# Performance work log

Hardware: AMD Instinct MI355X
Metric: run time of the kernel (lower is better)

Reference implementation:

```python
import jax, jax.numpy as jnp
import numpy as np

B, S, D, H, F, E = 8, 1024, 1024, 16, 3584, 2
HD = D // H
NUM_LABELS = 2
EPS = 1e-6


def setup_inputs() -> dict:
    key = jax.random.key(0)
    ks = jax.random.split(key, 10)
    w = lambda k, shape: jax.random.normal(k, shape, jnp.float32) * 0.02
    return {
        "hidden_states": jax.random.normal(ks[0], (B, S, D), jnp.float32),
        "ln1_w": jnp.ones((D,), jnp.float32),
        "q_w": w(ks[1], (D, D)),
        "k_w": w(ks[2], (D, D)),
        "v_w": w(ks[3], (D, D)),
        "o_w": w(ks[4], (D, D)),
        "ln2_w": jnp.ones((D,), jnp.float32),
        "router_w": w(ks[5], (D, E)),
        "gate_w": w(ks[6], (E, D, F)),
        "up_w": w(ks[7], (E, D, F)),
        "down_w": w(ks[8], (E, F, D)),
        "final_ln_w": jnp.ones((D,), jnp.float32),
        "score_w": w(ks[9], (D, NUM_LABELS)),
    }


def rmsnorm(x, w):
    var = jnp.mean(jnp.square(x), axis=-1, keepdims=True)
    return x * jax.lax.rsqrt(var + EPS) * w


def reference(hidden_states, ln1_w, q_w, k_w, v_w, o_w, ln2_w, router_w,
              gate_w, up_w, down_w, final_ln_w, score_w):
    x = hidden_states  # [B,S,D]
    # --- attention block (Jamba attention: no RoPE, no bias, causal) ---
    res = x
    h = rmsnorm(x, ln1_w)
    q = (h @ q_w).reshape(B, S, H, HD).transpose(0, 2, 1, 3)  # [B,H,S,HD]
    k = (h @ k_w).reshape(B, S, H, HD).transpose(0, 2, 1, 3)
    v = (h @ v_w).reshape(B, S, H, HD).transpose(0, 2, 1, 3)
    scores = jnp.einsum("bhqd,bhkd->bhqk", q, k) / np.sqrt(HD).astype(np.float32)
    causal = jnp.tril(jnp.ones((S, S), bool))
    scores = jnp.where(causal, scores, jnp.finfo(jnp.float32).min)
    attn = jax.nn.softmax(scores, axis=-1)
    ctx = jnp.einsum("bhqk,bhkd->bhqd", attn, v)
    attn_out = ctx.transpose(0, 2, 1, 3).reshape(B, S, D) @ o_w
    x = res + attn_out
    # --- top-1 MoE FFN (Jamba: softmax router, top-k, NO renormalization) ---
    res = x
    h = rmsnorm(x, ln2_w).reshape(B * S, D)
    router_logits = h @ router_w  # [N,E]
    probs = jax.nn.softmax(router_logits.astype(jnp.float32), axis=-1)
    top_w = jnp.max(probs, axis=-1)       # top-1 weight
    sel = jnp.argmax(probs, axis=-1)      # selected expert id
    moe = jnp.zeros_like(h)
    for e in range(E):  # fixed tiny loop over experts
        y = (jax.nn.silu(h @ gate_w[e]) * (h @ up_w[e])) @ down_w[e]
        moe = moe + jnp.where(sel == e, top_w, 0.0)[:, None] * y
    x = res + moe.reshape(B, S, D)
    # --- final RMSNorm + score head on first token ---
    x = rmsnorm(x, final_ln_w)
    logits = x[:, 0, :] @ score_w  # [B, NUM_LABELS]
    return logits
```

## Files before the change

kernel.cpp:

```cpp
#include <hip/hip_runtime.h>
#include <math.h>

#define B 8
#define S 1024
#define D 1024
#define F 3584

#define NBLK 256
#define KSV 64
#define CHV 16
#define KS5 16
#define CH5 64
#define KS6 112
#define CH6 32

#define LD4(p) (*(const float4*)(p))
#define FMA4(A, s, W) { (A).x += (s)*(W).x; (A).y += (s)*(W).y; (A).z += (s)*(W).z; (A).w += (s)*(W).w; }

#define BB8(bb, ACC, XS, CH, koff) { \
  float4 xa = LD4((XS) + (bb)*(CH) + (koff)); \
  float4 xb = LD4((XS) + (bb)*(CH) + (koff) + 4); \
  FMA4(ACC, xa.x, w0); FMA4(ACC, xa.y, w1); FMA4(ACC, xa.z, w2); FMA4(ACC, xa.w, w3); \
  FMA4(ACC, xb.x, w4); FMA4(ACC, xb.y, w5); FMA4(ACC, xb.z, w6); FMA4(ACC, xb.w, w7); }

#define ALL8(XS, CH, koff) \
  BB8(0, acc0, XS, CH, koff) BB8(1, acc1, XS, CH, koff) \
  BB8(2, acc2, XS, CH, koff) BB8(3, acc3, XS, CH, koff) \
  BB8(4, acc4, XS, CH, koff) BB8(5, acc5, XS, CH, koff) \
  BB8(6, acc6, XS, CH, koff) BB8(7, acc7, XS, CH, koff)

__device__ __forceinline__ float block_sum256(float v, volatile float* buf) {
  #pragma unroll
  for (int o = 32; o; o >>= 1) v += __shfl_down(v, o);
  __syncthreads();
  if ((threadIdx.x & 63) == 0) buf[threadIdx.x >> 6] = v;
  __syncthreads();
  return buf[0] + buf[1] + buf[2] + buf[3];
}

__device__ __forceinline__ void gsync(unsigned* bar, int phase) {
  __syncthreads();
  if (threadIdx.x == 0) {
    unsigned* flag = bar + 32 * phase;
    unsigned old = __hip_atomic_fetch_add(bar, 1u, __ATOMIC_ACQ_REL,
                                          __HIP_MEMORY_SCOPE_AGENT);
    if (old == (unsigned)(NBLK * phase) - 1u) {
      __hip_atomic_store(flag, 1u, __ATOMIC_RELEASE, __HIP_MEMORY_SCOPE_AGENT);
    } else {
      while (__hip_atomic_load(flag, __ATOMIC_RELAXED,
                               __HIP_MEMORY_SCOPE_AGENT) == 0u)
        __builtin_amdgcn_s_sleep(8);
      (void)__hip_atomic_load(flag, __ATOMIC_ACQUIRE, __HIP_MEMORY_SCOPE_AGENT);
    }
  }
  __syncthreads();
}

__device__ __forceinline__ void mv16(const float4* __restrict__ Wp,
                                     float* __restrict__ Pout,
                                     const float* xs, int j) {
  const int st = D / 4;
  float4 acc0 = {0,0,0,0}, acc1 = {0,0,0,0}, acc2 = {0,0,0,0}, acc3 = {0,0,0,0};
  float4 acc4 = {0,0,0,0}, acc5 = {0,0,0,0}, acc6 = {0,0,0,0}, acc7 = {0,0,0,0};
  float4 w0 = Wp[0*st], w1 = Wp[1*st], w2 = Wp[2*st], w3 = Wp[3*st];
  float4 w4 = Wp[4*st], w5 = Wp[5*st], w6 = Wp[6*st], w7 = Wp[7*st];
  float4 v0 = Wp[8*st], v1 = Wp[9*st], v2 = Wp[10*st], v3 = Wp[11*st];
  float4 v4 = Wp[12*st], v5 = Wp[13*st], v6 = Wp[14*st], v7 = Wp[15*st];
  ALL8(xs, CHV, 0);
  w0 = v0; w1 = v1; w2 = v2; w3 = v3; w4 = v4; w5 = v5; w6 = v6; w7 = v7;
  ALL8(xs, CHV, 8);
  *(float4*)(Pout + 0*(size_t)D + j) = acc0;
  *(float4*)(Pout + 1*(size_t)D + j) = acc1;
  *(float4*)(Pout + 2*(size_t)D + j) = acc2;
  *(float4*)(Pout + 3*(size_t)D + j) = acc3;
  *(float4*)(Pout + 4*(size_t)D + j) = acc4;
  *(float4*)(Pout + 5*(size_t)D + j) = acc5;
  *(float4*)(Pout + 6*(size_t)D + j) = acc6;
  *(float4*)(Pout + 7*(size_t)D + j) = acc7;
}

__global__ __launch_bounds__(256, 1) void k_fused(
    const float* __restrict__ hs, const float* __restrict__ ln1,
    const float* __restrict__ vw, const float* __restrict__ ow,
    const float* __restrict__ ln2, const float* __restrict__ rw,
    const float* __restrict__ gw, const float* __restrict__ uw,
    const float* __restrict__ dw, const float* __restrict__ flw,
    const float* __restrict__ sw, float* __restrict__ out,
    float* __restrict__ wsf, unsigned* __restrict__ bar) {
  __shared__ float xs[512];
  __shared__ float rbuf[4];
  const int tid = threadIdx.x;
  const int bid = blockIdx.x;

  float* h1    = wsf;
  float* Vp    = wsf + 8192;
  float* Op    = Vp + (size_t)KSV * 8 * D;
  float* xr    = Op + (size_t)KSV * 8 * D;
  float* h2    = xr + 8192;
  float* tw8   = h2 + 8192;
  int*   sel8  = (int*)(tw8 + 8);
  float* Pgu   = tw8 + 16;
  float* Dp    = Pgu + (size_t)KS5 * 4 * 8 * F;
  float* dummy = Dp + (size_t)KS6 * 2 * 8 * D;

  if (bid < 8) {
    int idx = tid * 4;
    float4 x = LD4(hs + (size_t)bid * S * D + idx);
    float ss = x.x*x.x + x.y*x.y + x.z*x.z + x.w*x.w;
    float tot = block_sum256(ss, rbuf);
    float sc = rsqrtf(tot * (1.f / (float)D) + 1e-6f);
    float4 wv = LD4(ln1 + idx);
    float4 o;
    o.x = x.x*sc*wv.x; o.y = x.y*sc*wv.y; o.z = x.z*sc*wv.z; o.w = x.w*sc*wv.w;
    *(float4*)(h1 + bid * D + idx) = o;
  }
  gsync(bar, 1);

  float4 pref = {0,0,0,0};

  if (bid < KSV) {
    int i0 = bid * CHV;
    if (tid < 128) xs[tid] = h1[(tid >> 4) * D + i0 + (tid & 15)];
    __syncthreads();
    int j = tid * 4;
    mv16((const float4*)(vw + (size_t)i0 * D + j), Vp + (size_t)bid * 8 * D, xs, j);
  } else {
    const float4* src = (const float4*)gw + (size_t)(bid - 64) * 4096 + tid;
    #pragma unroll
    for (int t = 0; t < 16; t++) {
      float4 v = src[(size_t)t * 256];
      pref.x += v.x; pref.y += v.y; pref.z += v.z; pref.w += v.w;
    }
  }
  gsync(bar, 2);

  if (bid < KSV) {
    int i0 = bid * CHV;
    if (tid < 128) {
      int bb = tid >> 4, ii = tid & 15;
      float s = 0.f;
      #pragma unroll 8
      for (int p = 0; p < KSV; p++) s += Vp[((size_t)p * 8 + bb) * D + i0 + ii];
      xs[bb * 16 + ii] = s;
    }
    __syncthreads();
    int j = tid * 4;
    mv16((const float4*)(ow + (size_t)i0 * D + j), Op + (size_t)bid * 8 * D, xs, j);
  } else {
    const float4* src = (const float4*)uw + (size_t)(bid - 64) * 4096 + tid;
    #pragma unroll
    for (int t = 0; t < 16; t++) {
      float4 v = src[(size_t)t * 256];
      pref.x += v.x; pref.y += v.y; pref.z += v.z; pref.w += v.w;
    }
    float tchk = pref.x + pref.y + pref.z + pref.w;
    if (tchk > 1e30f) dummy[bid] = tchk;
  }
  gsync(bar, 3);

  if (bid < 8) {
    int idx = tid * 4;
    float4 x = LD4(hs + (size_t)bid * S * D + idx);
    #pragma unroll 8
    for (int p = 0; p < KSV; p++) {
      float4 v = LD4(Op + ((size_t)p * 8 + bid) * D + idx);
      x.x += v.x; x.y += v.y; x.z += v.z; x.w += v.w;
    }
    *(float4*)(xr + bid * D + idx) = x;
    float ss = x.x*x.x + x.y*x.y + x.z*x.z + x.w*x.w;
    float tot = block_sum256(ss, rbuf);
    float sc = rsqrtf(tot * (1.f / (float)D) + 1e-6f);
    float4 wv = LD4(ln2 + idx);
    float4 h;
    h.x = x.x*sc*wv.x; h.y = x.y*sc*wv.y; h.z = x.z*sc*wv.z; h.w = x.w*sc*wv.w;
    *(float4*)(h2 + bid * D + idx) = h;
    float r0 = h.x * rw[idx * 2]     + h.y * rw[(idx + 1) * 2] +
               h.z * rw[(idx + 2) * 2] + h.w * rw[(idx + 3) * 2];
    float r1 = h.x * rw[idx * 2 + 1]     + h.y * rw[(idx + 1) * 2 + 1] +
               h.z * rw[(idx + 2) * 2 + 1] + h.w * rw[(idx + 3) * 2 + 1];
    r0 = block_sum256(r0, rbuf);
    r1 = block_sum256(r1, rbuf);
    if (tid == 0) {
      float m = fmaxf(r0, r1);
      float e0 = __expf(r0 - m), e1 = __expf(r1 - m);
      float inv = 1.f / (e0 + e1);
      float p0 = e0 * inv, p1 = e1 * inv;
      tw8[bid] = fmaxf(p0, p1);
      sel8[bid] = (p1 > p0) ? 1 : 0;
    }
  }
  gsync(bar, 4);

  if (bid < 14 * KS5) {
    int kc = bid & 15, colt = bid >> 4;
    int i0 = kc * CH5;
    { int bb = tid >> 6, r = tid & 63;
      xs[tid]       = h2[bb * D + i0 + r];
      xs[tid + 256] = h2[(bb + 4) * D + i0 + r]; }
    __syncthreads();
    int c = colt * 1024 + tid * 4;
    int m = c / F;
    int j = c - m * F;
    const float* base = (m < 2 ? gw : uw) + (size_t)(m & 1) * D * F;
    const float4* Wp = (const float4*)(base + (size_t)i0 * F + j);
    const int st = F / 4;
    float4 acc0 = {0,0,0,0}, acc1 = {0,0,0,0}, acc2 = {0,0,0,0}, acc3 = {0,0,0,0};
    float4 acc4 = {0,0,0,0}, acc5 = {0,0,0,0}, acc6 = {0,0,0,0}, acc7 = {0,0,0,0};
    float4 w0 = Wp[0*st], w1 = Wp[1*st], w2 = Wp[2*st], w3 = Wp[3*st];
    float4 w4 = Wp[4*st], w5 = Wp[5*st], w6 = Wp[6*st], w7 = Wp[7*st];
    Wp += 8 * st;
    #pragma unroll
    for (int t = 0; t < CH5 / 8 - 1; t++) {
      float4 n0 = Wp[0*st], n1 = Wp[1*st], n2 = Wp[2*st], n3 = Wp[3*st];
      float4 n4 = Wp[4*st], n5 = Wp[5*st], n6 = Wp[6*st], n7 = Wp[7*st];
      Wp += 8 * st;
      ALL8(xs, CH5, t * 8);
      w0 = n0; w1 = n1; w2 = n2; w3 = n3; w4 = n4; w5 = n5; w6 = n6; w7 = n7;
    }
    ALL8(xs, CH5, CH5 - 8);
    #define GU_ST(bb, ACC) \
      *(float4*)(Pgu + (((size_t)kc * 4 + m) * 8 + (bb)) * F + j) = ACC;
    GU_ST(0, acc0) GU_ST(1, acc1) GU_ST(2, acc2) GU_ST(3, acc3)
    GU_ST(4, acc4) GU_ST(5, acc5) GU_ST(6, acc6) GU_ST(7, acc7)
    #undef GU_ST
  }
  gsync(bar, 5);

  if (bid < 2 * KS6) {
    int e = bid & 1, ch = bid >> 1, i0 = ch * CH6;
    { int bb = tid >> 5, ii = tid & 31;
      float ga = 0.f, ua = 0.f;
      #pragma unroll
      for (int kc = 0; kc < KS5; kc++) {
        ga += Pgu[(((size_t)kc * 4 + e)     * 8 + bb) * F + i0 + ii];
        ua += Pgu[(((size_t)kc * 4 + 2 + e) * 8 + bb) * F + i0 + ii];
      }
      xs[bb * CH6 + ii] = (ga / (1.f + __expf(-ga))) * ua; }
    __syncthreads();
    int j = tid * 4;
    const float4* Wp = (const float4*)(dw + (size_t)e * F * D + (size_t)i0 * D + j);
    const int st = D / 4;
    float4 acc0 = {0,0,0,0}, acc1 = {0,0,0,0}, acc2 = {0,0,0,0}, acc3 = {0,0,0,0};
    float4 acc4 = {0,0,0,0}, acc5 = {0,0,0,0}, acc6 = {0,0,0,0}, acc7 = {0,0,0,0};
    float4 w0 = Wp[0*st], w1 = Wp[1*st], w2 = Wp[2*st], w3 = Wp[3*st];
    float4 w4 = Wp[4*st], w5 = Wp[5*st], w6 = Wp[6*st], w7 = Wp[7*st];
    Wp += 8 * st;
    #pragma unroll
    for (int t = 0; t < CH6 / 8 - 1; t++) {
      float4 n0 = Wp[0*st], n1 = Wp[1*st], n2 = Wp[2*st], n3 = Wp[3*st];
      float4 n4 = Wp[4*st], n5 = Wp[5*st], n6 = Wp[6*st], n7 = Wp[7*st];
      Wp += 8 * st;
      ALL8(xs, CH6, t * 8);
      w0 = n0; w1 = n1; w2 = n2; w3 = n3; w4 = n4; w5 = n5; w6 = n6; w7 = n7;
    }
    ALL8(xs, CH6, CH6 - 8);
    #define DN_ST(bb, ACC) \
      *(float4*)(Dp + (((size_t)ch * 2 + e) * 8 + (bb)) * D + j) = ACC;
    DN_ST(0, acc0) DN_ST(1, acc1) DN_ST(2, acc2) DN_ST(3, acc3)
    DN_ST(4, acc4) DN_ST(5, acc5) DN_ST(6, acc6) DN_ST(7, acc7)
    #undef DN_ST
  }
  gsync(bar, 6);

  if (bid < 8) {
    int e = sel8[bid];
    float tw = tw8[bid];
    int idx = tid * 4;
    float4 y = {0,0,0,0};
    #pragma unroll 8
    for (int p = 0; p < KS6; p++) {
      float4 v = LD4(Dp + (((size_t)p * 2 + e) * 8 + bid) * D + idx);
      y.x += v.x; y.y += v.y; y.z += v.z; y.w += v.w;
    }
    float4 x = LD4(xr + bid * D + idx);
    x.x += tw * y.x; x.y += tw * y.y; x.z += tw * y.z; x.w += tw * y.w;
    float ss = x.x*x.x + x.y*x.y + x.z*x.z + x.w*x.w;
    float tot = block_sum256(ss, rbuf);
    float sc = rsqrtf(tot * (1.f / (float)D) + 1e-6f);
    float4 wv = LD4(flw + idx);
    float n0 = x.x*sc*wv.x, n1 = x.y*sc*wv.y, n2 = x.z*sc*wv.z, n3 = x.w*sc*wv.w;
    float l0 = n0 * sw[idx * 2]     + n1 * sw[(idx + 1) * 2] +
               n2 * sw[(idx + 2) * 2] + n3 * sw[(idx + 3) * 2];
    float l1 = n0 * sw[idx * 2 + 1]     + n1 * sw[(idx + 1) * 2 + 1] +
               n2 * sw[(idx + 2) * 2 + 1] + n3 * sw[(idx + 3) * 2 + 1];
    l0 = block_sum256(l0, rbuf);
    l1 = block_sum256(l1, rbuf);
    if (tid == 0) { out[bid * 2 + 0] = l0; out[bid * 2 + 1] = l1; }
  }
}

extern "C" void kernel_launch(void* const* d_in, const int* in_sizes, int n_in,
                              void* d_out, int out_size, void* d_ws, size_t ws_size,
                              hipStream_t stream) {
  const float* hs  = (const float*)d_in[0];
  const float* ln1 = (const float*)d_in[1];
  const float* vw  = (const float*)d_in[4];
  const float* ow  = (const float*)d_in[5];
  const float* ln2 = (const float*)d_in[6];
  const float* rw  = (const float*)d_in[7];
  const float* gw  = (const float*)d_in[8];
  const float* uw  = (const float*)d_in[9];
  const float* dw  = (const float*)d_in[10];
  const float* flw = (const float*)d_in[11];
  const float* sw  = (const float*)d_in[12];

  unsigned* bar = (unsigned*)d_ws;
  float* wsf = (float*)d_ws + 256;

  (void)hipMemsetAsync(d_ws, 0, 1024, stream);
  hipLaunchKernelGGL(k_fused, dim3(NBLK), dim3(256), 0, stream,
                     hs, ln1, vw, ow, ln2, rw, gw, uw, dw, flw, sw,
                     (float*)d_out, wsf, bar);
}
```

Baseline: 252.2 us.

## Split persistent grid-synced kernel into six separate launches

Replaces the single persistent kernel with hand-rolled atomic grid barriers by six kernels launched back to back on the stream. The idle-block weight prefetch of gate/up weights is dropped, and RMSNorm-1 is folded into the V projection kernel. Gate/up and down kernels now skip storing partial results for experts a row did not select. The change trades barrier spin costs for kernel-launch gaps and loses the L2 prefetch overlap.

```diff
diff --git a/kernel.cpp b/kernel.cpp
--- a/kernel.cpp
+++ b/kernel.cpp
@@ -6,7 +6,6 @@
 #define D 1024
 #define F 3584
 
-#define NBLK 256
 #define KSV 64
 #define CHV 16
 #define KS5 16
@@ -36,24 +35,6 @@
   if ((threadIdx.x & 63) == 0) buf[threadIdx.x >> 6] = v;
   __syncthreads();
   return buf[0] + buf[1] + buf[2] + buf[3];
-}
-
-__device__ __forceinline__ void gsync(unsigned* bar, int phase) {
-  __syncthreads();
-  if (threadIdx.x == 0) {
-    unsigned* flag = bar + 32 * phase;
-    unsigned old = __hip_atomic_fetch_add(bar, 1u, __ATOMIC_ACQ_REL,
-                                          __HIP_MEMORY_SCOPE_AGENT);
-    if (old == (unsigned)(NBLK * phase) - 1u) {
-      __hip_atomic_store(flag, 1u, __ATOMIC_RELEASE, __HIP_MEMORY_SCOPE_AGENT);
-    } else {
-      while (__hip_atomic_load(flag, __ATOMIC_RELAXED,
-                               __HIP_MEMORY_SCOPE_AGENT) == 0u)
-        __builtin_amdgcn_s_sleep(8);
-      (void)__hip_atomic_load(flag, __ATOMIC_ACQUIRE, __HIP_MEMORY_SCOPE_AGENT);
-    }
-  }
-  __syncthreads();
 }
 
 __device__ __forceinline__ void mv16(const float4* __restrict__ Wp,
@@ -79,214 +60,215 @@
   *(float4*)(Pout + 7*(size_t)D + j) = acc7;
 }
 
-__global__ __launch_bounds__(256, 1) void k_fused(
-    const float* __restrict__ hs, const float* __restrict__ ln1,
-    const float* __restrict__ vw, const float* __restrict__ ow,
-    const float* __restrict__ ln2, const float* __restrict__ rw,
-    const float* __restrict__ gw, const float* __restrict__ uw,
-    const float* __restrict__ dw, const float* __restrict__ flw,
-    const float* __restrict__ sw, float* __restrict__ out,
-    float* __restrict__ wsf, unsigned* __restrict__ bar) {
-  __shared__ float xs[512];
-  __shared__ float rbuf[4];
-  const int tid = threadIdx.x;
-  const int bid = blockIdx.x;
-
-  float* h1    = wsf;
-  float* Vp    = wsf + 8192;
-  float* Op    = Vp + (size_t)KSV * 8 * D;
-  float* xr    = Op + (size_t)KSV * 8 * D;
-  float* h2    = xr + 8192;
-  float* tw8   = h2 + 8192;
-  int*   sel8  = (int*)(tw8 + 8);
-  float* Pgu   = tw8 + 16;
-  float* Dp    = Pgu + (size_t)KS5 * 4 * 8 * F;
-  float* dummy = Dp + (size_t)KS6 * 2 * 8 * D;
-
-  if (bid < 8) {
-    int idx = tid * 4;
-    float4 x = LD4(hs + (size_t)bid * S * D + idx);
-    float ss = x.x*x.x + x.y*x.y + x.z*x.z + x.w*x.w;
-    float tot = block_sum256(ss, rbuf);
-    float sc = rsqrtf(tot * (1.f / (float)D) + 1e-6f);
-    float4 wv = LD4(ln1 + idx);
-    float4 o;
-    o.x = x.x*sc*wv.x; o.y = x.y*sc*wv.y; o.z = x.z*sc*wv.z; o.w = x.w*sc*wv.w;
-    *(float4*)(h1 + bid * D + idx) = o;
-  }
-  gsync(bar, 1);
-
-  float4 pref = {0,0,0,0};
-
-  if (bid < KSV) {
-    int i0 = bid * CHV;
-    if (tid < 128) xs[tid] = h1[(tid >> 4) * D + i0 + (tid & 15)];
-    __syncthreads();
-    int j = tid * 4;
-    mv16((const float4*)(vw + (size_t)i0 * D + j), Vp + (size_t)bid * 8 * D, xs, j);
-  } else {
-    const float4* src = (const float4*)gw + (size_t)(bid - 64) * 4096 + tid;
+__global__ __launch_bounds__(256, 2) void k_mvp_v(const float* __restrict__ hs,
+                                                  const float* __restrict__ ln1w,
+                                                  const float* __restrict__ vw,
+                                                  float* __restrict__ Vp) {
+  __shared__ float xs[8 * CHV];
+  __shared__ float scsh[8];
+  int tid = threadIdx.x;
+  int w = tid >> 6, lane = tid & 63;
+  #pragma unroll
+  for (int b2 = 0; b2 < 2; b2++) {
+    int b = w * 2 + b2;
+    const float4* hp = (const float4*)(hs + (size_t)b * S * D);
+    float ss = 0.f;
     #pragma unroll
-    for (int t = 0; t < 16; t++) {
-      float4 v = src[(size_t)t * 256];
-      pref.x += v.x; pref.y += v.y; pref.z += v.z; pref.w += v.w;
+    for (int t = 0; t < 4; t++) {
+      float4 v = hp[lane * 4 + t];
+      ss += v.x*v.x + v.y*v.y + v.z*v.z + v.w*v.w;
     }
-  }
-  gsync(bar, 2);
-
-  if (bid < KSV) {
-    int i0 = bid * CHV;
-    if (tid < 128) {
-      int bb = tid >> 4, ii = tid & 15;
-      float s = 0.f;
-      #pragma unroll 8
-      for (int p = 0; p < KSV; p++) s += Vp[((size_t)p * 8 + bb) * D + i0 + ii];
-      xs[bb * 16 + ii] = s;
-    }
-    __syncthreads();
-    int j = tid * 4;
-    mv16((const float4*)(ow + (size_t)i0 * D + j), Op + (size_t)bid * 8 * D, xs, j);
-  } else {
-    const float4* src = (const float4*)uw + (size_t)(bid - 64) * 4096 + tid;
     #pragma unroll
-    for (int t = 0; t < 16; t++) {
-      float4 v = src[(size_t)t * 256];
-      pref.x += v.x; pref.y += v.y; pref.z += v.z; pref.w += v.w;
-    }
-    float tchk = pref.x + pref.y + pref.z + pref.w;
-    if (tchk > 1e30f) dummy[bid] = tchk;
-  }
-  gsync(bar, 3);
-
-  if (bid < 8) {
-    int idx = tid * 4;
-    float4 x = LD4(hs + (size_t)bid * S * D + idx);
-    #pragma unroll 8
-    for (int p = 0; p < KSV; p++) {
-      float4 v = LD4(Op + ((size_t)p * 8 + bid) * D + idx);
-      x.x += v.x; x.y += v.y; x.z += v.z; x.w += v.w;
-    }
-    *(float4*)(xr + bid * D + idx) = x;
-    float ss = x.x*x.x + x.y*x.y + x.z*x.z + x.w*x.w;
-    float tot = block_sum256(ss, rbuf);
-    float sc = rsqrtf(tot * (1.f / (float)D) + 1e-6f);
-    float4 wv = LD4(ln2 + idx);
-    float4 h;
-    h.x = x.x*sc*wv.x; h.y = x.y*sc*wv.y; h.z = x.z*sc*wv.z; h.w = x.w*sc*wv.w;
-    *(float4*)(h2 + bid * D + idx) = h;
-    float r0 = h.x * rw[idx * 2]     + h.y * rw[(idx + 1) * 2] +
-               h.z * rw[(idx + 2) * 2] + h.w * rw[(idx + 3) * 2];
-    float r1 = h.x * rw[idx * 2 + 1]     + h.y * rw[(idx + 1) * 2 + 1] +
-               h.z * rw[(idx + 2) * 2 + 1] + h.w * rw[(idx + 3) * 2 + 1];
-    r0 = block_sum256(r0, rbuf);
-    r1 = block_sum256(r1, rbuf);
-    if (tid == 0) {
-      float m = fmaxf(r0, r1);
-      float e0 = __expf(r0 - m), e1 = __expf(r1 - m);
-      float inv = 1.f / (e0 + e1);
-      float p0 = e0 * inv, p1 = e1 * inv;
-      tw8[bid] = fmaxf(p0, p1);
-      sel8[bid] = (p1 > p0) ? 1 : 0;
-    }
-  }
-  gsync(bar, 4);
-
-  if (bid < 14 * KS5) {
-    int kc = bid & 15, colt = bid >> 4;
-    int i0 = kc * CH5;
-    { int bb = tid >> 6, r = tid & 63;
-      xs[tid]       = h2[bb * D + i0 + r];
-      xs[tid + 256] = h2[(bb + 4) * D + i0 + r]; }
-    __syncthreads();
-    int c = colt * 1024 + tid * 4;
-    int m = c / F;
-    int j = c - m * F;
-    const float* base = (m < 2 ? gw : uw) + (size_t)(m & 1) * D * F;
-    const float4* Wp = (const float4*)(base + (size_t)i0 * F + j);
-    const int st = F / 4;
-    float4 acc0 = {0,0,0,0}, acc1 = {0,0,0,0}, acc2 = {0,0,0,0}, acc3 = {0,0,0,0};
-    float4 acc4 = {0,0,0,0}, acc5 = {0,0,0,0}, acc6 = {0,0,0,0}, acc7 = {0,0,0,0};
-    float4 w0 = Wp[0*st], w1 = Wp[1*st], w2 = Wp[2*st], w3 = Wp[3*st];
-    float4 w4 = Wp[4*st], w5 = Wp[5*st], w6 = Wp[6*st], w7 = Wp[7*st];
+    for (int o = 32; o; o >>= 1) ss += __shfl_down(ss, o);
+    if (lane == 0) scsh[b] = rsqrtf(ss * (1.f / (float)D) + 1e-6f);
+  }
+  __syncthreads();
+  int i0 = blockIdx.x * CHV;
+  if (tid < 128) {
+    int bb = tid >> 4, ii = tid & 15;
+    xs[tid] = hs[(size_t)bb * S * D + i0 + ii] * scsh[bb] * ln1w[i0 + ii];
+  }
+  __syncthreads();
+  int j = tid * 4;
+  mv16((const float4*)(vw + (size_t)i0 * D + j), Vp + (size_t)blockIdx.x * 8 * D, xs, j);
+}
+
+__global__ __launch_bounds__(256, 2) void k_ored(const float* __restrict__ Vp,
+                                                 const float* __restrict__ ow,
+                                                 float* __restrict__ Op) {
+  __shared__ float xs[8 * CHV];
+  int tid = threadIdx.x;
+  int i0 = blockIdx.x * CHV;
+  if (tid < 128) {
+    int bb = tid >> 4, ii = tid & 15;
+    float s = 0.f;
+    #pragma unroll 16
+    for (int p = 0; p < KSV; p++) s += Vp[((size_t)p * 8 + bb) * D + i0 + ii];
+    xs[bb * CHV + ii] = s;
+  }
+  __syncthreads();
+  int j = tid * 4;
+  mv16((const float4*)(ow + (size_t)i0 * D + j), Op + (size_t)blockIdx.x * 8 * D, xs, j);
+}
+
+__global__ void k_mid(const float* __restrict__ hs, const float* __restrict__ Op,
+                      const float* __restrict__ ln2, const float* __restrict__ rw,
+                      float* __restrict__ xr, float* __restrict__ h2,
+                      float* __restrict__ topw, int* __restrict__ sel) {
+  __shared__ float buf[4];
+  int b = blockIdx.x;
+  int idx = threadIdx.x * 4;
+  float4 x = LD4(hs + (size_t)b * S * D + idx);
+  #pragma unroll 16
+  for (int p = 0; p < KSV; p++) {
+    float4 v = LD4(Op + ((size_t)p * 8 + b) * D + idx);
+    x.x += v.x; x.y += v.y; x.z += v.z; x.w += v.w;
+  }
+  *(float4*)(xr + b * D + idx) = x;
+  float ss = x.x*x.x + x.y*x.y + x.z*x.z + x.w*x.w;
+  float tot = block_sum256(ss, buf);
+  float sc = rsqrtf(tot * (1.f / (float)D) + 1e-6f);
+  float4 wv = LD4(ln2 + idx);
+  float4 h;
+  h.x = x.x*sc*wv.x; h.y = x.y*sc*wv.y; h.z = x.z*sc*wv.z; h.w = x.w*sc*wv.w;
+  *(float4*)(h2 + b * D + idx) = h;
+  float r0 = h.x * rw[idx * 2]     + h.y * rw[(idx + 1) * 2] +
+             h.z * rw[(idx + 2) * 2] + h.w * rw[(idx + 3) * 2];
+  float r1 = h.x * rw[idx * 2 + 1]     + h.y * rw[(idx + 1) * 2 + 1] +
+             h.z * rw[(idx + 2) * 2 + 1] + h.w * rw[(idx + 3) * 2 + 1];
+  r0 = block_sum256(r0, buf);
+  r1 = block_sum256(r1, buf);
+  if (threadIdx.x == 0) {
+    float m = fmaxf(r0, r1);
+    float e0 = __expf(r0 - m), e1 = __expf(r1 - m);
+    float inv = 1.f / (e0 + e1);
+    float p0 = e0 * inv, p1 = e1 * inv;
+    topw[b] = fmaxf(p0, p1);
+    sel[b] = (p1 > p0) ? 1 : 0;
+  }
+}
+
+__global__ __launch_bounds__(256, 2) void k_gateup(const float* __restrict__ h2,
+                                                   const float* __restrict__ gw,
+                                                   const float* __restrict__ uw,
+                                                   const int* __restrict__ sel,
+                                                   float* __restrict__ Pgu) {
+  __shared__ float xs[8 * CH5];
+  __shared__ int ssel[8];
+  int tid = threadIdx.x;
+  int kc = blockIdx.y, colt = blockIdx.x;
+  int i0 = kc * CH5;
+  { int bb = tid >> 6, r = tid & 63;
+    xs[tid]       = h2[bb * D + i0 + r];
+    xs[tid + 256] = h2[(bb + 4) * D + i0 + r]; }
+  if (tid < 8) ssel[tid] = sel[tid];
+  __syncthreads();
+  int c = colt * 1024 + tid * 4;
+  int m = c / F;
+  int j = c - m * F;
+  const float* base = (m < 2 ? gw : uw) + (size_t)(m & 1) * D * F;
+  const float4* Wp = (const float4*)(base + (size_t)i0 * F + j);
+  const int st = F / 4;
+  float4 acc0 = {0,0,0,0}, acc1 = {0,0,0,0}, acc2 = {0,0,0,0}, acc3 = {0,0,0,0};
+  float4 acc4 = {0,0,0,0}, acc5 = {0,0,0,0}, acc6 = {0,0,0,0}, acc7 = {0,0,0,0};
+  float4 w0 = Wp[0*st], w1 = Wp[1*st], w2 = Wp[2*st], w3 = Wp[3*st];
+  float4 w4 = Wp[4*st], w5 = Wp[5*st], w6 = Wp[6*st], w7 = Wp[7*st];
+  Wp += 8 * st;
+  #pragma unroll
+  for (int t = 0; t < CH5 / 8 - 1; t++) {
+    float4 n0 = Wp[0*st], n1 = Wp[1*st], n2 = Wp[2*st], n3 = Wp[3*st];
+    float4 n4 = Wp[4*st], n5 = Wp[5*st], n6 = Wp[6*st], n7 = Wp[7*st];
     Wp += 8 * st;
-    #pragma unroll
-    for (int t = 0; t < CH5 / 8 - 1; t++) {
-      float4 n0 = Wp[0*st], n1 = Wp[1*st], n2 = Wp[2*st], n3 = Wp[3*st];
-      float4 n4 = Wp[4*st], n5 = Wp[5*st], n6 = Wp[6*st], n7 = Wp[7*st];
-      Wp += 8 * st;
-      ALL8(xs, CH5, t * 8);
-      w0 = n0; w1 = n1; w2 = n2; w3 = n3; w4 = n4; w5 = n5; w6 = n6; w7 = n7;
-    }
-    ALL8(xs, CH5, CH5 - 8);
-    #define GU_ST(bb, ACC) \
+    ALL8(xs, CH5, t * 8);
+    w0 = n0; w1 = n1; w2 = n2; w3 = n3; w4 = n4; w5 = n5; w6 = n6; w7 = n7;
+  }
+  ALL8(xs, CH5, CH5 - 8);
+  int me = m & 1;
+  #define GU_ST(bb, ACC) \
+    if (ssel[bb] == me) \
       *(float4*)(Pgu + (((size_t)kc * 4 + m) * 8 + (bb)) * F + j) = ACC;
-    GU_ST(0, acc0) GU_ST(1, acc1) GU_ST(2, acc2) GU_ST(3, acc3)
-    GU_ST(4, acc4) GU_ST(5, acc5) GU_ST(6, acc6) GU_ST(7, acc7)
-    #undef GU_ST
-  }
-  gsync(bar, 5);
-
-  if (bid < 2 * KS6) {
-    int e = bid & 1, ch = bid >> 1, i0 = ch * CH6;
-    { int bb = tid >> 5, ii = tid & 31;
+  GU_ST(0, acc0) GU_ST(1, acc1) GU_ST(2, acc2) GU_ST(3, acc3)
+  GU_ST(4, acc4) GU_ST(5, acc5) GU_ST(6, acc6) GU_ST(7, acc7)
+  #undef GU_ST
+}
+
+__global__ __launch_bounds__(256, 2) void k_down(const float* __restrict__ Pgu,
+                                                 const float* __restrict__ dw,
+                                                 const int* __restrict__ sel,
+                                                 float* __restrict__ Dp) {
+  __shared__ float xs[8 * CH6];
+  __shared__ int ssel[8];
+  int tid = threadIdx.x;
+  int e = blockIdx.x & 1, ch = blockIdx.x >> 1, i0 = ch * CH6;
+  if (tid < 8) ssel[tid] = sel[tid];
+  __syncthreads();
+  { int bb = tid >> 5, ii = tid & 31;
+    float r = 0.f;
+    if (ssel[bb] == e) {
       float ga = 0.f, ua = 0.f;
       #pragma unroll
       for (int kc = 0; kc < KS5; kc++) {
         ga += Pgu[(((size_t)kc * 4 + e)     * 8 + bb) * F + i0 + ii];
         ua += Pgu[(((size_t)kc * 4 + 2 + e) * 8 + bb) * F + i0 + ii];
       }
-      xs[bb * CH6 + ii] = (ga / (1.f + __expf(-ga))) * ua; }
-    __syncthreads();
-    int j = tid * 4;
-    const float4* Wp = (const float4*)(dw + (size_t)e * F * D + (size_t)i0 * D + j);
-    const int st = D / 4;
-    float4 acc0 = {0,0,0,0}, acc1 = {0,0,0,0}, acc2 = {0,0,0,0}, acc3 = {0,0,0,0};
-    float4 acc4 = {0,0,0,0}, acc5 = {0,0,0,0}, acc6 = {0,0,0,0}, acc7 = {0,0,0,0};
-    float4 w0 = Wp[0*st], w1 = Wp[1*st], w2 = Wp[2*st], w3 = Wp[3*st];
-    float4 w4 = Wp[4*st], w5 = Wp[5*st], w6 = Wp[6*st], w7 = Wp[7*st];
+      r = (ga / (1.f + __expf(-ga))) * ua;
+    }
+    xs[bb * CH6 + ii] = r; }
+  __syncthreads();
+  int j = tid * 4;
+  const float4* Wp = (const float4*)(dw + (size_t)e * F * D + (size_t)i0 * D + j);
+  const int st = D / 4;
+  float4 acc0 = {0,0,0,0}, acc1 = {0,0,0,0}, acc2 = {0,0,0,0}, acc3 = {0,0,0,0};
+  float4 acc4 = {0,0,0,0}, acc5 = {0,0,0,0}, acc6 = {0,0,0,0}, acc7 = {0,0,0,0};
+  float4 w0 = Wp[0*st], w1 = Wp[1*st], w2 = Wp[2*st], w3 = Wp[3*st];
+  float4 w4 = Wp[4*st], w5 = Wp[5*st], w6 = Wp[6*st], w7 = Wp[7*st];
+  Wp += 8 * st;
+  #pragma unroll
+  for (int t = 0; t < CH6 / 8 - 1; t++) {
+    float4 n0 = Wp[0*st], n1 = Wp[1*st], n2 = Wp[2*st], n3 = Wp[3*st];
+    float4 n4 = Wp[4*st], n5 = Wp[5*st], n6 = Wp[6*st], n7 = Wp[7*st];
     Wp += 8 * st;
-    #pragma unroll
-    for (int t = 0; t < CH6 / 8 - 1; t++) {
-      float4 n0 = Wp[0*st], n1 = Wp[1*st], n2 = Wp[2*st], n3 = Wp[3*st];
-      float4 n4 = Wp[4*st], n5 = Wp[5*st], n6 = Wp[6*st], n7 = Wp[7*st];
-      Wp += 8 * st;
-      ALL8(xs, CH6, t * 8);
-      w0 = n0; w1 = n1; w2 = n2; w3 = n3; w4 = n4; w5 = n5; w6 = n6; w7 = n7;
-    }
-    ALL8(xs, CH6, CH6 - 8);
-    #define DN_ST(bb, ACC) \
+    ALL8(xs, CH6, t * 8);
+    w0 = n0; w1 = n1; w2 = n2; w3 = n3; w4 = n4; w5 = n5; w6 = n6; w7 = n7;
+  }
+  ALL8(xs, CH6, CH6 - 8);
+  #define DN_ST(bb, ACC) \
+    if (ssel[bb] == e) \
       *(float4*)(Dp + (((size_t)ch * 2 + e) * 8 + (bb)) * D + j) = ACC;
-    DN_ST(0, acc0) DN_ST(1, acc1) DN_ST(2, acc2) DN_ST(3, acc3)
-    DN_ST(4, acc4) DN_ST(5, acc5) DN_ST(6, acc6) DN_ST(7, acc7)
-    #undef DN_ST
-  }
-  gsync(bar, 6);
-
-  if (bid < 8) {
-    int e = sel8[bid];
-    float tw = tw8[bid];
-    int idx = tid * 4;
-    float4 y = {0,0,0,0};
-    #pragma unroll 8
-    for (int p = 0; p < KS6; p++) {
-      float4 v = LD4(Dp + (((size_t)p * 2 + e) * 8 + bid) * D + idx);
-      y.x += v.x; y.y += v.y; y.z += v.z; y.w += v.w;
-    }
-    float4 x = LD4(xr + bid * D + idx);
-    x.x += tw * y.x; x.y += tw * y.y; x.z += tw * y.z; x.w += tw * y.w;
-    float ss = x.x*x.x + x.y*x.y + x.z*x.z + x.w*x.w;
-    float tot = block_sum256(ss, rbuf);
-    float sc = rsqrtf(tot * (1.f / (float)D) + 1e-6f);
-    float4 wv = LD4(flw + idx);
-    float n0 = x.x*sc*wv.x, n1 = x.y*sc*wv.y, n2 = x.z*sc*wv.z, n3 = x.w*sc*wv.w;
-    float l0 = n0 * sw[idx * 2]     + n1 * sw[(idx + 1) * 2] +
-               n2 * sw[(idx + 2) * 2] + n3 * sw[(idx + 3) * 2];
-    float l1 = n0 * sw[idx * 2 + 1]     + n1 * sw[(idx + 1) * 2 + 1] +
-               n2 * sw[(idx + 2) * 2 + 1] + n3 * sw[(idx + 3) * 2 + 1];
-    l0 = block_sum256(l0, rbuf);
-    l1 = block_sum256(l1, rbuf);
-    if (tid == 0) { out[bid * 2 + 0] = l0; out[bid * 2 + 1] = l1; }
-  }
+  DN_ST(0, acc0) DN_ST(1, acc1) DN_ST(2, acc2) DN_ST(3, acc3)
+  DN_ST(4, acc4) DN_ST(5, acc5) DN_ST(6, acc6) DN_ST(7, acc7)
+  #undef DN_ST
+}
+
+__global__ void k_final(const float* __restrict__ xr, const float* __restrict__ Dp,
+                        const float* __restrict__ topw, const int* __restrict__ sel,
+                        const float* __restrict__ flw, const float* __restrict__ sw,
+                        float* __restrict__ out) {
+  __shared__ float buf[4];
+  int b = blockIdx.x;
+  int e = sel[b];
+  float tw = topw[b];
+  int idx = threadIdx.x * 4;
+  float4 y = {0,0,0,0};
+  #pragma unroll 16
+  for (int p = 0; p < KS6; p++) {
+    float4 v = LD4(Dp + (((size_t)p * 2 + e) * 8 + b) * D + idx);
+    y.x += v.x; y.y += v.y; y.z += v.z; y.w += v.w;
+  }
+  float4 x = LD4(xr + b * D + idx);
+  x.x += tw * y.x; x.y += tw * y.y; x.z += tw * y.z; x.w += tw * y.w;
+  float ss = x.x*x.x + x.y*x.y + x.z*x.z + x.w*x.w;
+  float tot = block_sum256(ss, buf);
+  float sc = rsqrtf(tot * (1.f / (float)D) + 1e-6f);
+  float4 wv = LD4(flw + idx);
+  float n0 = x.x*sc*wv.x, n1 = x.y*sc*wv.y, n2 = x.z*sc*wv.z, n3 = x.w*sc*wv.w;
+  float l0 = n0 * sw[idx * 2]     + n1 * sw[(idx + 1) * 2] +
+             n2 * sw[(idx + 2) * 2] + n3 * sw[(idx + 3) * 2];
+  float l1 = n0 * sw[idx * 2 + 1]     + n1 * sw[(idx + 1) * 2 + 1] +
+             n2 * sw[(idx + 2) * 2 + 1] + n3 * sw[(idx + 3) * 2 + 1];
+  l0 = block_sum256(l0, buf);
+  l1 = block_sum256(l1, buf);
+  if (threadIdx.x == 0) { out[b * 2 + 0] = l0; out[b * 2 + 1] = l1; }
 }
 
 extern "C" void kernel_launch(void* const* d_in, const int* in_sizes, int n_in,
@@ -304,11 +286,20 @@
   const float* flw = (const float*)d_in[11];
   const float* sw  = (const float*)d_in[12];
 
-  unsigned* bar = (unsigned*)d_ws;
-  float* wsf = (float*)d_ws + 256;
-
-  (void)hipMemsetAsync(d_ws, 0, 1024, stream);
-  hipLaunchKernelGGL(k_fused, dim3(NBLK), dim3(256), 0, stream,
-                     hs, ln1, vw, ow, ln2, rw, gw, uw, dw, flw, sw,
-                     (float*)d_out, wsf, bar);
-}
+  float* ws = (float*)d_ws;
+  float* Vp   = ws;
+  float* Op   = Vp + 524288;
+  float* xr   = Op + 524288;
+  float* h2   = xr + 8192;
+  float* tw8  = h2 + 8192;
+  int*   sel8 = (int*)(tw8 + 8);
+  float* Pgu  = tw8 + 16;
+  float* Dp   = Pgu + 1835008;
+
+  k_mvp_v<<<KSV, 256, 0, stream>>>(hs, ln1, vw, Vp);
+  k_ored<<<KSV, 256, 0, stream>>>(Vp, ow, Op);
+  k_mid<<<8, 256, 0, stream>>>(hs, Op, ln2, rw, xr, h2, tw8, sel8);
+  k_gateup<<<dim3(14, KS5), 256, 0, stream>>>(h2, gw, uw, sel8, Pgu);
+  k_down<<<2 * KS6, 256, 0, stream>>>(Pgu, dw, sel8, Dp);
+  k_final<<<8, 256, 0, stream>>>(xr, Dp, tw8, sel8, flw, sw, (float*)d_out);
+}
```

Result: slower. 258.1 us (+2.4%).
